# Performance work log

Hardware: AMD Instinct MI355X
Metric: run time of the kernel (lower is better)

## Reference

```python
import jax, jax.numpy as jnp
import numpy as np

B, S, NS, MAX_W, H, NH = 4, 512, 8192, 16, 256, 4
DH = H // NH
FF = 4 * H
NEG = -1e9  # finite mask value; fully-padded spans are zeroed at the end anyway


def _layernorm(x, g, b, eps=1e-5):
    m = jnp.mean(x, -1, keepdims=True)
    v = jnp.var(x, -1, keepdims=True)
    return (x - m) * jax.lax.rsqrt(v + eps) * g + b


def _pos_encoding(n, d):
    pos = np.arange(n)[:, None]
    div = np.exp(np.arange(0, d, 2) * (-np.log(10000.0) / d))
    pe = np.zeros((n, d), np.float32)
    pe[:, 0::2] = np.sin(pos * div)
    pe[:, 1::2] = np.cos(pos * div)
    return jnp.asarray(pe)


def setup_inputs():
    key = jax.random.key(0)
    ks = jax.random.split(key, 12)
    sc = 1.0 / np.sqrt(H)
    starts = jax.random.randint(ks[1], (B, NS), 0, S - MAX_W)
    lengths = jax.random.randint(ks[2], (B, NS), 1, MAX_W + 1)
    return {
        "token_reps": jax.random.normal(ks[0], (B, S, H), jnp.float32),
        "span_ids": jnp.stack([starts, starts + lengths], -1),
        "span_masks": jax.random.uniform(ks[3], (B, NS)) < 0.9,
        "pooling": 1,
        "dummy_query": jax.random.normal(ks[4], (H,), jnp.float32) * sc,
        "w_q": jax.random.normal(ks[5], (H, H), jnp.float32) * sc,
        "w_k": jax.random.normal(ks[6], (H, H), jnp.float32) * sc,
        "w_v": jax.random.normal(ks[7], (H, H), jnp.float32) * sc,
        "b_qkv": jnp.zeros((3, H), jnp.float32),
        "w_o": jax.random.normal(ks[8], (H, H), jnp.float32) * sc,
        "b_o": jnp.zeros((H,), jnp.float32),
        "ln_g": jnp.ones((H,), jnp.float32),
        "ln_b": jnp.zeros((H,), jnp.float32),
        "ffn_w1": jax.random.normal(ks[9], (H, FF), jnp.float32) * sc,
        "ffn_b1": jnp.zeros((FF,), jnp.float32),
        "ffn_w2": jax.random.normal(ks[10], (FF, H), jnp.float32) * (1.0 / np.sqrt(FF)),
        "ffn_b2": jnp.zeros((H,), jnp.float32),
    }


def reference(token_reps, span_ids, span_masks, pooling, dummy_query, w_q, w_k, w_v,
              b_qkv, w_o, b_o, ln_g, ln_b, ffn_w1, ffn_b1, ffn_w2, ffn_b2):
    # sequence positional encoding (eval mode -> dropout is identity)
    tr = token_reps + _pos_encoding(S, H)[None]  # [B,S,H]
    # span lengths, zeroed where span is masked out (as in torch code)
    span_len = (span_ids[:, :, 1] - span_ids[:, :, 0]) * span_masks.astype(span_ids.dtype)  # [B,NS]
    offs = jnp.arange(MAX_W)
    valid = offs[None, None, :] < span_len[:, :, None]  # [B,NS,W] True = real token
    pos = jnp.clip(span_ids[:, :, 0:1] + offs[None, None, :], 0, S - 1)  # [B,NS,W]
    # vectorized ragged gather replacing the python double loop
    x = tr[jnp.arange(B)[:, None, None], pos]  # [B,NS,W,H]
    x = jnp.where(valid[..., None], x, 0.0)
    # single-query multi-head cross attention (dummy query attends over span tokens)
    q = (dummy_query @ w_q.T + b_qkv[0]).reshape(NH, DH)
    k = (x @ w_k.T + b_qkv[1]).reshape(B, NS, MAX_W, NH, DH)
    v = (x @ w_v.T + b_qkv[2]).reshape(B, NS, MAX_W, NH, DH)
    logits = jnp.einsum('hd,bnwhd->bnhw', q, k) / np.sqrt(DH)
    logits = jnp.where(valid[:, :, None, :], logits, NEG)
    attn = jax.nn.softmax(logits, axis=-1)
    ctx = jnp.einsum('bnhw,bnwhd->bnhd', attn, v).reshape(B, NS, H)
    out = ctx @ w_o.T + b_o + dummy_query  # residual with the dummy query
    y = _layernorm(out, ln_g, ln_b)
    f = jax.nn.relu(y @ ffn_w1 + ffn_b1) @ ffn_w2 + ffn_b2
    y = _layernorm(f + y, ln_g, ln_b)
    return jnp.where(span_masks[..., None], y, 0.0)  # [B,NS,H]
```

## Files before the change

### kernel.cpp

```cpp
#include <hip/hip_runtime.h>
#include <hip/hip_bf16.h>

#define B_    4
#define S_    512
#define NS_   8192
#define MAXW  16
#define H_    256
#define NH_   4
#define FF_   1024
#define NSPAN (B_*NS_)
#define NEGV  (-1.0e9f)
#define MT    64
#define LDSK  264

typedef short s16x8 __attribute__((ext_vector_type(8)));
typedef float f32x4 __attribute__((ext_vector_type(4)));

__device__ __forceinline__ unsigned short f2bu(float v){
  __hip_bfloat16 h = __float2bfloat16(v);
  union { __hip_bfloat16 h; unsigned short u; } c; c.h = h; return c.u;
}
__device__ __forceinline__ float bu2f(unsigned short u){
  union { unsigned int i; float f; } c; c.i = ((unsigned int)u) << 16; return c.f;
}
__device__ __forceinline__ f32x4 MFMA(s16x8 a, s16x8 b, f32x4 c){
  return __builtin_amdgcn_mfma_f32_16x16x32_bf16(a, b, c, 0, 0, 0);
}

__global__ __launch_bounds__(256) void prep_q_kernel(
    const float* __restrict__ dq, const float* __restrict__ wq,
    const float* __restrict__ wk, const float* __restrict__ bqkv,
    float* __restrict__ qkvec, float* __restrict__ qb)
{
  __shared__ float q_s[H_];
  const int t = threadIdx.x;
  const int h = blockIdx.x;
  float acc = bqkv[t];
  const float4* wr = (const float4*)(wq + (size_t)t*H_);
  #pragma unroll 8
  for (int c = 0; c < 64; ++c) {
    float4 u = wr[c];
    float4 d = *(const float4*)(dq + c*4);
    acc += u.x*d.x + u.y*d.y + u.z*d.z + u.w*d.w;
  }
  q_s[t] = acc;
  __syncthreads();
  float s = 0.f;
  #pragma unroll 8
  for (int d = 0; d < 64; ++d) s += q_s[h*64 + d] * wk[(size_t)(h*64 + d)*H_ + t];
  qkvec[h*H_ + t] = s;
  if (t < 64) {
    float p = q_s[h*64 + t] * bqkv[H_ + h*64 + t];
    #pragma unroll
    for (int off = 32; off; off >>= 1) p += __shfl_down(p, off);
    if (t == 0) qb[h] = p;
  }
}

__global__ __launch_bounds__(256) void prep_all_kernel(
    const float* __restrict__ tok, const float* __restrict__ qkvec,
    const float* __restrict__ qb,
    const float* __restrict__ wv, const float* __restrict__ wo,
    const float* __restrict__ bqkv, const float* __restrict__ bo,
    const float* __restrict__ dq,
    const float* __restrict__ w1, const float* __restrict__ w2,
    unsigned short* __restrict__ trbf,
    float* __restrict__ lt, unsigned short* __restrict__ wct,
    unsigned short* __restrict__ w1t, unsigned short* __restrict__ w2t,
    float* __restrict__ zbias)
{
  const int blk = blockIdx.x;
  const int t = threadIdx.x;
  if (blk < 2048) {
    __shared__ float red[4][4];
    const int row = blk;
    const int p = row & (S_ - 1);
    float fac = expf((float)((t >> 1)*2) * (-9.210340371976184f / 256.0f));
    float ang = (float)p * fac;
    float pe = (t & 1) ? cosf(ang) : sinf(ang);
    float v = tok[(size_t)row*H_ + t] + pe;
    trbf[(size_t)row*H_ + t] = f2bu(v);
    float p0 = qkvec[t]*v, p1 = qkvec[H_+t]*v, p2 = qkvec[2*H_+t]*v, p3 = qkvec[3*H_+t]*v;
    const int l = t & 63, wv_ = t >> 6;
    #pragma unroll
    for (int m = 1; m < 64; m <<= 1) {
      p0 += __shfl_xor(p0, m); p1 += __shfl_xor(p1, m);
      p2 += __shfl_xor(p2, m); p3 += __shfl_xor(p3, m);
    }
    if (l == 0) { red[wv_][0]=p0; red[wv_][1]=p1; red[wv_][2]=p2; red[wv_][3]=p3; }
    __syncthreads();
    if (t < 4)
      lt[row*NH_ + t] = (red[0][t]+red[1][t]+red[2][t]+red[3][t] + qb[t]) * 0.125f;
  } else if (blk < 3072) {
    int idx = (blk - 2048)*256 + t;
    int n = idx >> 8, k = idx & 255;
    w1t[idx] = f2bu(w1[(size_t)k*FF_ + n]);
  } else if (blk < 4096) {
    int idx = (blk - 3072)*256 + t;
    int n = idx >> 10, k = idx & 1023;
    w2t[idx] = f2bu(w2[(size_t)k*H_ + n]);
  } else if (blk < 4352) {
    __shared__ float wo_s[H_];
    const int i = blk - 4096;
    wo_s[t] = wo[(size_t)i*H_ + t];
    __syncthreads();
    #pragma unroll
    for (int h = 0; h < NH_; ++h) {
      float s = 0.f;
      #pragma unroll 8
      for (int d = 0; d < 64; ++d)
        s += wo_s[h*64 + d] * wv[(size_t)(h*64 + d)*H_ + t];
      wct[(size_t)i*1024 + h*H_ + t] = f2bu(s);
    }
  } else {
    __shared__ float bv_s[H_];
    bv_s[t] = bqkv[2*H_ + t];
    __syncthreads();
    float acc = bo[t] + dq[t];
    const float4* wr = (const float4*)(wo + (size_t)t*H_);
    #pragma unroll 8
    for (int c = 0; c < 64; ++c) {
      float4 u = wr[c];
      acc += u.x*bv_s[c*4] + u.y*bv_s[c*4+1] + u.z*bv_s[c*4+2] + u.w*bv_s[c*4+3];
    }
    zbias[t] = acc;
  }
}

__global__ __launch_bounds__(256) void pool_kernel(
    const unsigned short* __restrict__ trbf,
    const float* __restrict__ lt,
    const int* __restrict__ span_ids, const int* __restrict__ span_masks,
    int span0, unsigned short* __restrict__ pooled)
{
  const int t = threadIdx.x;
  const int l = t & 63;
  const int wv = t >> 6;
  const int spanL = blockIdx.x * 4 + wv;
  const int span  = span0 + spanL;
  const int b  = span >> 13;
  const int st = span_ids[span*2];
  const int en = span_ids[span*2 + 1];
  const int len = span_masks[span] ? (en - st) : 0;

  const int h = l >> 4, w = l & 15;
  int pos = st + w; pos = pos < 0 ? 0 : (pos > S_-1 ? S_-1 : pos);
  float logit = (w < len) ? lt[(b*S_ + pos)*NH_ + h] : NEGV;
  float mx = logit;
  mx = fmaxf(mx, __shfl_xor(mx, 1));
  mx = fmaxf(mx, __shfl_xor(mx, 2));
  mx = fmaxf(mx, __shfl_xor(mx, 4));
  mx = fmaxf(mx, __shfl_xor(mx, 8));
  float e = expf(logit - mx);
  float se = e;
  se += __shfl_xor(se, 1); se += __shfl_xor(se, 2);
  se += __shfl_xor(se, 4); se += __shfl_xor(se, 8);
  const float av = e / se;

  float acc[NH_][4];
  #pragma unroll
  for (int hh = 0; hh < NH_; ++hh)
    #pragma unroll
    for (int j = 0; j < 4; ++j) acc[hh][j] = 0.f;

  const unsigned short* rb = trbf + (size_t)(b*S_)*H_ + l*4;
  #pragma unroll
  for (int w2 = 0; w2 < MAXW; ++w2) {
    int p2 = st + w2; p2 = p2 < 0 ? 0 : (p2 > S_-1 ? S_-1 : p2);
    ushort4 xv = *(const ushort4*)(rb + (size_t)p2*H_);
    float x0 = bu2f(xv.x), x1 = bu2f(xv.y), x2 = bu2f(xv.z), x3 = bu2f(xv.w);
    #pragma unroll
    for (int hh = 0; hh < NH_; ++hh) {
      float a = __shfl(av, hh*16 + w2);
      acc[hh][0] += a*x0; acc[hh][1] += a*x1;
      acc[hh][2] += a*x2; acc[hh][3] += a*x3;
    }
  }
  unsigned short* pp = pooled + (size_t)spanL * 1024;
  #pragma unroll
  for (int hh = 0; hh < NH_; ++hh) {
    ushort4 o;
    o.x = f2bu(acc[hh][0]); o.y = f2bu(acc[hh][1]);
    o.z = f2bu(acc[hh][2]); o.w = f2bu(acc[hh][3]);
    *(ushort4*)(pp + hh*256 + l*4) = o;
  }
}

__device__ __forceinline__ void gemm8(const unsigned short* __restrict__ As,
                                      const unsigned short* __restrict__ bp0,
                                      const unsigned short* __restrict__ bp1,
                                      f32x4 (&ac)[4][2], int ln16, int lg)
{
  s16x8 B0 = *(const s16x8*)bp0;
  s16x8 B1 = *(const s16x8*)bp1;
  #pragma unroll
  for (int s = 0; s < 8; ++s) {
    s16x8 N0 = B0, N1 = B1;
    if (s < 7) { N0 = *(const s16x8*)(bp0 + (s+1)*32); N1 = *(const s16x8*)(bp1 + (s+1)*32); }
    s16x8 a0 = *(const s16x8*)(As + (0*16+ln16)*LDSK + s*32 + lg*8);
    s16x8 a1 = *(const s16x8*)(As + (1*16+ln16)*LDSK + s*32 + lg*8);
    s16x8 a2 = *(const s16x8*)(As + (2*16+ln16)*LDSK + s*32 + lg*8);
    s16x8 a3 = *(const s16x8*)(As + (3*16+ln16)*LDSK + s*32 + lg*8);
    ac[0][0]=MFMA(a0,B0,ac[0][0]); ac[1][0]=MFMA(a1,B0,ac[1][0]);
    ac[2][0]=MFMA(a2,B0,ac[2][0]); ac[3][0]=MFMA(a3,B0,ac[3][0]);
    ac[0][1]=MFMA(a0,B1,ac[0][1]); ac[1][1]=MFMA(a1,B1,ac[1][1]);
    ac[2][1]=MFMA(a2,B1,ac[2][1]); ac[3][1]=MFMA(a3,B1,ac[3][1]);
    B0 = N0; B1 = N1;
  }
}

__global__ __launch_bounds__(512, 4) void fused_gemm_kernel(
    const unsigned short* __restrict__ pooled,
    const unsigned short* __restrict__ wct,
    const float* __restrict__ zbias,
    const unsigned short* __restrict__ w1t, const float* __restrict__ b1,
    const unsigned short* __restrict__ w2t, const float* __restrict__ b2,
    const float* __restrict__ lng, const float* __restrict__ lnb,
    const int* __restrict__ masks, int span0,
    float* __restrict__ out)
{
  __shared__ __align__(16) unsigned short bufA[MT][LDSK];
  __shared__ __align__(16) unsigned short bufB[MT][LDSK];
  __shared__ float part_s[8][MT][2];

  const int t = threadIdx.x;
  const int l = t & 63;
  const int w = t >> 6;
  const int ln16 = l & 15;
  const int lg = l >> 4;
  const int m0l = blockIdx.x * MT;
  const int m0g = span0 + m0l;
  const int ncol = w * 32;

  int srow[4], k8[4];
  #pragma unroll
  for (int q = 0; q < 4; ++q) {
    int idx = q*512 + t;
    srow[q] = idx >> 5;
    k8[q]   = (idx & 31)*8;
  }
  const unsigned short* pbase = pooled + (size_t)m0l*1024;

  f32x4 acc[4][2];
  #pragma unroll
  for (int mf = 0; mf < 4; ++mf){ acc[mf][0]=(f32x4){0,0,0,0}; acc[mf][1]=(f32x4){0,0,0,0}; }

  const unsigned short* bz0 = wct + (size_t)(ncol + ln16)*1024 + lg*8;
  const unsigned short* bz1 = wct + (size_t)(ncol + 16 + ln16)*1024 + lg*8;

  unsigned short* As = &bufA[0][0];
  unsigned short* An = &bufB[0][0];

  uint4 sr[4];
  #pragma unroll
  for (int q = 0; q < 4; ++q)
    sr[q] = *(const uint4*)(pbase + (size_t)srow[q]*1024 + k8[q]);
  #pragma unroll
  for (int q = 0; q < 4; ++q)
    *(uint4*)(As + srow[q]*LDSK + k8[q]) = sr[q];
  __syncthreads();

  s16x8 GA[4], GB[4];
  #define LOADBZ(G, kkg) { \
    G[0] = *(const s16x8*)(bz0 + (kkg)*64);      \
    G[1] = *(const s16x8*)(bz0 + (kkg)*64 + 32); \
    G[2] = *(const s16x8*)(bz1 + (kkg)*64);      \
    G[3] = *(const s16x8*)(bz1 + (kkg)*64 + 32); }
  LOADBZ(GA, 0); LOADBZ(GB, 1);

  auto zstep = [&](s16x8 (&G)[4], int kk, int kkgnext) {
    #pragma unroll
    for (int half = 0; half < 2; ++half) {
      s16x8 a0 = *(const s16x8*)(As + (0*16+ln16)*LDSK + kk*64 + half*32 + lg*8);
      s16x8 a1 = *(const s16x8*)(As + (1*16+ln16)*LDSK + kk*64 + half*32 + lg*8);
      s16x8 a2 = *(const s16x8*)(As + (2*16+ln16)*LDSK + kk*64 + half*32 + lg*8);
      s16x8 a3 = *(const s16x8*)(As + (3*16+ln16)*LDSK + kk*64 + half*32 + lg*8);
      acc[0][0]=MFMA(a0,G[0+half],acc[0][0]); acc[1][0]=MFMA(a1,G[0+half],acc[1][0]);
      acc[2][0]=MFMA(a2,G[0+half],acc[2][0]); acc[3][0]=MFMA(a3,G[0+half],acc[3][0]);
      acc[0][1]=MFMA(a0,G[2+half],acc[0][1]); acc[1][1]=MFMA(a1,G[2+half],acc[1][1]);
      acc[2][1]=MFMA(a2,G[2+half],acc[2][1]); acc[3][1]=MFMA(a3,G[2+half],acc[3][1]);
    }
    if (kkgnext < 16) LOADBZ(G, kkgnext);
  };

  #pragma unroll
  for (int c = 0; c < 4; ++c) {
    if (c < 3) {
      #pragma unroll
      for (int q = 0; q < 4; ++q)
        sr[q] = *(const uint4*)(pbase + (size_t)srow[q]*1024 + (c+1)*256 + k8[q]);
    }
    zstep(GA, 0, c*4 + 2);
    zstep(GB, 1, c*4 + 3);
    zstep(GA, 2, c*4 + 4);
    zstep(GB, 3, c*4 + 5);
    if (c < 3) {
      #pragma unroll
      for (int q = 0; q < 4; ++q)
        *(uint4*)(An + srow[q]*LDSK + k8[q]) = sr[q];
      __syncthreads();
      unsigned short* tmp = As; As = An; An = tmp;
    }
  }
  #undef LOADBZ

  unsigned short* y_s  = &bufB[0][0];
  unsigned short* f1_s = &bufA[0][0];
  {
    const float zb0 = zbias[ncol + ln16],      zb1 = zbias[ncol + 16 + ln16];
    const float g0  = lng[ncol + ln16],        g1  = lng[ncol + 16 + ln16];
    const float bl0 = lnb[ncol + ln16],        bl1 = lnb[ncol + 16 + ln16];
    float vals[4][4][2];
    #pragma unroll
    for (int mf = 0; mf < 4; ++mf)
      #pragma unroll
      for (int r = 0; r < 4; ++r) {
        const int row = mf*16 + lg*4 + r;
        float v0 = acc[mf][0][r] + zb0;
        float v1 = acc[mf][1][r] + zb1;
        vals[mf][r][0] = v0; vals[mf][r][1] = v1;
        float s1 = v0 + v1, s2 = v0*v0 + v1*v1;
        s1 += __shfl_xor(s1,1); s2 += __shfl_xor(s2,1);
        s1 += __shfl_xor(s1,2); s2 += __shfl_xor(s2,2);
        s1 += __shfl_xor(s1,4); s2 += __shfl_xor(s2,4);
        s1 += __shfl_xor(s1,8); s2 += __shfl_xor(s2,8);
        if (ln16 == 0) { part_s[w][row][0] = s1; part_s[w][row][1] = s2; }
      }
    __syncthreads();
    #pragma unroll
    for (int mf = 0; mf < 4; ++mf)
      #pragma unroll
      for (int r = 0; r < 4; ++r) {
        const int row = mf*16 + lg*4 + r;
        float s1 = 0.f, s2 = 0.f;
        #pragma unroll
        for (int j = 0; j < 8; ++j) { s1 += part_s[j][row][0]; s2 += part_s[j][row][1]; }
        float mean = s1 * (1.f/H_);
        float var  = s2 * (1.f/H_) - mean*mean; var = fmaxf(var, 0.f);
        float rstd = rsqrtf(var + 1e-5f);
        y_s[row*LDSK + ncol + ln16]      = f2bu((vals[mf][r][0]-mean)*rstd*g0 + bl0);
        y_s[row*LDSK + ncol + 16 + ln16] = f2bu((vals[mf][r][1]-mean)*rstd*g1 + bl1);
      }
  }
  __syncthreads();

  f32x4 f2acc[4][2];
  #pragma unroll
  for (int mf = 0; mf < 4; ++mf){ f2acc[mf][0]=(f32x4){0,0,0,0}; f2acc[mf][1]=(f32x4){0,0,0,0}; }

  #pragma unroll 1
  for (int nc = 0; nc < 4; ++nc) {
    #pragma unroll
    for (int mf = 0; mf < 4; ++mf){ acc[mf][0]=(f32x4){0,0,0,0}; acc[mf][1]=(f32x4){0,0,0,0}; }
    const unsigned short* b10 = w1t + (size_t)(nc*256 + ncol + ln16)*256 + lg*8;
    const unsigned short* b11 = w1t + (size_t)(nc*256 + ncol + 16 + ln16)*256 + lg*8;
    gemm8(y_s, b10, b11, acc, ln16, lg);
    __syncthreads();
    {
      const float bb0 = b1[nc*256 + ncol + ln16];
      const float bb1 = b1[nc*256 + ncol + 16 + ln16];
      #pragma unroll
      for (int mf = 0; mf < 4; ++mf)
        #pragma unroll
        for (int r = 0; r < 4; ++r) {
          const int row = mf*16 + lg*4 + r;
          f1_s[row*LDSK + ncol + ln16]      = f2bu(fmaxf(acc[mf][0][r] + bb0, 0.f));
          f1_s[row*LDSK + ncol + 16 + ln16] = f2bu(fmaxf(acc[mf][1][r] + bb1, 0.f));
        }
    }
    __syncthreads();
    const unsigned short* b20 = w2t + (size_t)(ncol + ln16)*1024 + nc*256 + lg*8;
    const unsigned short* b21 = w2t + (size_t)(ncol + 16 + ln16)*1024 + nc*256 + lg*8;
    gemm8(f1_s, b20, b21, f2acc, ln16, lg);
  }

  {
    const float b20v = b2[ncol + ln16],   b21v = b2[ncol + 16 + ln16];
    const float g0   = lng[ncol + ln16],  g1   = lng[ncol + 16 + ln16];
    const float bl0  = lnb[ncol + ln16],  bl1  = lnb[ncol + 16 + ln16];
    float vals[4][4][2];
    #pragma unroll
    for (int mf = 0; mf < 4; ++mf)
      #pragma unroll
      for (int r = 0; r < 4; ++r) {
        const int row = mf*16 + lg*4 + r;
        float v0 = f2acc[mf][0][r] + b20v + bu2f(y_s[row*LDSK + ncol + ln16]);
        float v1 = f2acc[mf][1][r] + b21v + bu2f(y_s[row*LDSK + ncol + 16 + ln16]);
        vals[mf][r][0] = v0; vals[mf][r][1] = v1;
        float s1 = v0 + v1, s2 = v0*v0 + v1*v1;
        s1 += __shfl_xor(s1,1); s2 += __shfl_xor(s2,1);
        s1 += __shfl_xor(s1,2); s2 += __shfl_xor(s2,2);
        s1 += __shfl_xor(s1,4); s2 += __shfl_xor(s2,4);
        s1 += __shfl_xor(s1,8); s2 += __shfl_xor(s2,8);
        if (ln16 == 0) { part_s[w][row][0] = s1; part_s[w][row][1] = s2; }
      }
    __syncthreads();
    #pragma unroll
    for (int mf = 0; mf < 4; ++mf)
      #pragma unroll
      for (int r = 0; r < 4; ++r) {
        const int row = mf*16 + lg*4 + r;
        const int span = m0g + row;
        float s1 = 0.f, s2 = 0.f;
        #pragma unroll
        for (int j = 0; j < 8; ++j) { s1 += part_s[j][row][0]; s2 += part_s[j][row][1]; }
        float mean = s1 * (1.f/H_);
        float var  = s2 * (1.f/H_) - mean*mean; var = fmaxf(var, 0.f);
        float rstd = rsqrtf(var + 1e-5f);
        int mk = masks[span];
        float o0 = (vals[mf][r][0]-mean)*rstd*g0 + bl0;
        float o1 = (vals[mf][r][1]-mean)*rstd*g1 + bl1;
        out[(size_t)span*H_ + ncol + ln16]      = mk ? o0 : 0.f;
        out[(size_t)span*H_ + ncol + 16 + ln16] = mk ? o1 : 0.f;
      }
  }
}

extern "C" void kernel_launch(void* const* d_in, const int* in_sizes, int n_in,
                              void* d_out, int out_size, void* d_ws, size_t ws_size,
                              hipStream_t stream) {
  const float* tok      = (const float*)d_in[0];
  const int* span_ids   = (const int*)d_in[1];
  const int* span_masks = (const int*)d_in[2];
  const float* dq   = (const float*)d_in[4];
  const float* wq   = (const float*)d_in[5];
  const float* wk   = (const float*)d_in[6];
  const float* wv   = (const float*)d_in[7];
  const float* bqkv = (const float*)d_in[8];
  const float* wo   = (const float*)d_in[9];
  const float* bo   = (const float*)d_in[10];
  const float* lng  = (const float*)d_in[11];
  const float* lnb  = (const float*)d_in[12];
  const float* w1   = (const float*)d_in[13];
  const float* b1   = (const float*)d_in[14];
  const float* w2   = (const float*)d_in[15];
  const float* b2   = (const float*)d_in[16];

  float* ws    = (float*)d_ws;
  float* qkvec = ws;
  float* qbuf  = qkvec + 1024;
  float* lt    = qbuf + 8;
  float* zbias = lt + 8192;
  unsigned short* ub = (unsigned short*)(zbias + 256);
  unsigned short* trbf = ub;
  unsigned short* wct  = trbf + 524288;
  unsigned short* w1t  = wct + 262144;
  unsigned short* w2t  = w1t + 262144;
  unsigned short* pooled = w2t + 262144;

  const size_t fixed_bytes = (size_t)(1024 + 8 + 8192 + 256)*4
                           + (size_t)(524288 + 262144*3)*2;
  int nb = 1;
  while (nb < 16 && fixed_bytes + (size_t)(NSPAN/nb)*1024*2 > ws_size) nb <<= 1;
  const int spans_b = NSPAN / nb;

  hipLaunchKernelGGL(prep_q_kernel, dim3(NH_), dim3(256), 0, stream,
                     dq, wq, wk, bqkv, qkvec, qbuf);
  hipLaunchKernelGGL(prep_all_kernel, dim3(4353), dim3(256), 0, stream,
                     tok, qkvec, qbuf, wv, wo, bqkv, bo, dq, w1, w2,
                     trbf, lt, wct, w1t, w2t, zbias);

  for (int bi = 0; bi < nb; ++bi) {
    const int span0 = bi * spans_b;
    hipLaunchKernelGGL(pool_kernel, dim3(spans_b/4), dim3(256), 0, stream,
                       trbf, lt, span_ids, span_masks, span0, pooled);
    hipLaunchKernelGGL(fused_gemm_kernel, dim3(spans_b/MT), dim3(512), 0, stream,
                       pooled, wct, zbias, w1t, b1, w2t, b2,
                       lng, lnb, span_masks, span0, (float*)d_out);
  }
}
```

Before: 175.6 us.

## Fuse span attention pooling into the fused GEMM kernel via shared memory

Removes the separate pool kernel and its global pooled buffer of 32768x1024 bf16. Each GEMM block now computes the per-span softmax weights and the attention-weighted token sums for two heads at a time straight into shared memory, then runs the Wct GEMM on them. This removes a global write and read of the pooled intermediate, plus a kernel launch and any batching loop. In exchange the GEMM block does extra gather work with more syncs, and shared memory use grows, which may lower occupancy.

```diff
diff --git a/kernel.cpp b/kernel.cpp
--- a/kernel.cpp
+++ b/kernel.cpp
@@ -127,65 +127,6 @@
   }
 }
 
-__global__ __launch_bounds__(256) void pool_kernel(
-    const unsigned short* __restrict__ trbf,
-    const float* __restrict__ lt,
-    const int* __restrict__ span_ids, const int* __restrict__ span_masks,
-    int span0, unsigned short* __restrict__ pooled)
-{
-  const int t = threadIdx.x;
-  const int l = t & 63;
-  const int wv = t >> 6;
-  const int spanL = blockIdx.x * 4 + wv;
-  const int span  = span0 + spanL;
-  const int b  = span >> 13;
-  const int st = span_ids[span*2];
-  const int en = span_ids[span*2 + 1];
-  const int len = span_masks[span] ? (en - st) : 0;
-
-  const int h = l >> 4, w = l & 15;
-  int pos = st + w; pos = pos < 0 ? 0 : (pos > S_-1 ? S_-1 : pos);
-  float logit = (w < len) ? lt[(b*S_ + pos)*NH_ + h] : NEGV;
-  float mx = logit;
-  mx = fmaxf(mx, __shfl_xor(mx, 1));
-  mx = fmaxf(mx, __shfl_xor(mx, 2));
-  mx = fmaxf(mx, __shfl_xor(mx, 4));
-  mx = fmaxf(mx, __shfl_xor(mx, 8));
-  float e = expf(logit - mx);
-  float se = e;
-  se += __shfl_xor(se, 1); se += __shfl_xor(se, 2);
-  se += __shfl_xor(se, 4); se += __shfl_xor(se, 8);
-  const float av = e / se;
-
-  float acc[NH_][4];
-  #pragma unroll
-  for (int hh = 0; hh < NH_; ++hh)
-    #pragma unroll
-    for (int j = 0; j < 4; ++j) acc[hh][j] = 0.f;
-
-  const unsigned short* rb = trbf + (size_t)(b*S_)*H_ + l*4;
-  #pragma unroll
-  for (int w2 = 0; w2 < MAXW; ++w2) {
-    int p2 = st + w2; p2 = p2 < 0 ? 0 : (p2 > S_-1 ? S_-1 : p2);
-    ushort4 xv = *(const ushort4*)(rb + (size_t)p2*H_);
-    float x0 = bu2f(xv.x), x1 = bu2f(xv.y), x2 = bu2f(xv.z), x3 = bu2f(xv.w);
-    #pragma unroll
-    for (int hh = 0; hh < NH_; ++hh) {
-      float a = __shfl(av, hh*16 + w2);
-      acc[hh][0] += a*x0; acc[hh][1] += a*x1;
-      acc[hh][2] += a*x2; acc[hh][3] += a*x3;
-    }
-  }
-  unsigned short* pp = pooled + (size_t)spanL * 1024;
-  #pragma unroll
-  for (int hh = 0; hh < NH_; ++hh) {
-    ushort4 o;
-    o.x = f2bu(acc[hh][0]); o.y = f2bu(acc[hh][1]);
-    o.z = f2bu(acc[hh][2]); o.w = f2bu(acc[hh][3]);
-    *(ushort4*)(pp + hh*256 + l*4) = o;
-  }
-}
-
 __device__ __forceinline__ void gemm8(const unsigned short* __restrict__ As,
                                       const unsigned short* __restrict__ bp0,
                                       const unsigned short* __restrict__ bp1,
@@ -210,106 +151,119 @@
 }
 
 __global__ __launch_bounds__(512, 4) void fused_gemm_kernel(
-    const unsigned short* __restrict__ pooled,
-    const unsigned short* __restrict__ wct,
-    const float* __restrict__ zbias,
+    const unsigned short* __restrict__ trbf, const float* __restrict__ lt,
+    const int* __restrict__ span_ids, const int* __restrict__ span_masks,
+    const unsigned short* __restrict__ wct, const float* __restrict__ zbias,
     const unsigned short* __restrict__ w1t, const float* __restrict__ b1,
     const unsigned short* __restrict__ w2t, const float* __restrict__ b2,
     const float* __restrict__ lng, const float* __restrict__ lnb,
-    const int* __restrict__ masks, int span0,
     float* __restrict__ out)
 {
-  __shared__ __align__(16) unsigned short bufA[MT][LDSK];
-  __shared__ __align__(16) unsigned short bufB[MT][LDSK];
-  __shared__ float part_s[8][MT][2];
+  __shared__ __align__(16) unsigned short bufA[MT*LDSK];
+  __shared__ __align__(16) unsigned short bufB[MT*LDSK];
+  __shared__ __align__(16) float scratch[2048];
+  __shared__ int meta_rb[MT];
+  __shared__ int meta_len[MT];
+  __shared__ int meta_mk[MT];
+
+  float (*attn_s)[MT][16] = (float(*)[MT][16])scratch;
+  float (*part_s)[MT][2]  = (float(*)[MT][2])scratch;
 
   const int t = threadIdx.x;
   const int l = t & 63;
   const int w = t >> 6;
   const int ln16 = l & 15;
   const int lg = l >> 4;
-  const int m0l = blockIdx.x * MT;
-  const int m0g = span0 + m0l;
+  const int m0 = blockIdx.x * MT;
   const int ncol = w * 32;
 
-  int srow[4], k8[4];
-  #pragma unroll
-  for (int q = 0; q < 4; ++q) {
-    int idx = q*512 + t;
-    srow[q] = idx >> 5;
-    k8[q]   = (idx & 31)*8;
-  }
-  const unsigned short* pbase = pooled + (size_t)m0l*1024;
+  if (t < MT) {
+    int gs = m0 + t;
+    int st = span_ids[gs*2];
+    int en = span_ids[gs*2 + 1];
+    int mk = span_masks[gs];
+    meta_rb[t]  = (gs >> 13) * S_ + st;
+    meta_len[t] = mk ? (en - st) : 0;
+    meta_mk[t]  = mk;
+  }
+  __syncthreads();
+
+  auto attn_pass = [&](int p){
+    #pragma unroll
+    for (int q = 0; q < 4; ++q) {
+      int slot = q*512 + t;
+      int w16 = slot & 15;
+      int sp  = (slot >> 4) & 63;
+      int h2  = slot >> 10;
+      int rb  = meta_rb[sp];
+      int len = meta_len[sp];
+      float lg_ = (w16 < len) ? lt[(rb + w16)*NH_ + p*2 + h2] : NEGV;
+      float mx = lg_;
+      mx = fmaxf(mx, __shfl_xor(mx,1));
+      mx = fmaxf(mx, __shfl_xor(mx,2));
+      mx = fmaxf(mx, __shfl_xor(mx,4));
+      mx = fmaxf(mx, __shfl_xor(mx,8));
+      float e = expf(lg_ - mx);
+      float se = e;
+      se += __shfl_xor(se,1); se += __shfl_xor(se,2);
+      se += __shfl_xor(se,4); se += __shfl_xor(se,8);
+      attn_s[h2][sp][w16] = e / se;
+    }
+  };
+
+  auto pool_pass = [&](){
+    #pragma unroll 1
+    for (int i = 0; i < 8; ++i) {
+      int sp = w*8 + i;
+      int rb = meta_rb[sp];
+      const ushort4* p4 = (const ushort4*)(trbf + (size_t)rb*H_) + l;
+      float a0=0,a1=0,a2=0,a3=0, q0=0,q1=0,q2=0,q3=0;
+      #pragma unroll
+      for (int w2 = 0; w2 < MAXW; ++w2) {
+        ushort4 xv = p4[w2*64];
+        float av0 = attn_s[0][sp][w2];
+        float av1 = attn_s[1][sp][w2];
+        float x0=bu2f(xv.x), x1=bu2f(xv.y), x2=bu2f(xv.z), x3=bu2f(xv.w);
+        a0 += av0*x0; a1 += av0*x1; a2 += av0*x2; a3 += av0*x3;
+        q0 += av1*x0; q1 += av1*x1; q2 += av1*x2; q3 += av1*x3;
+      }
+      ushort4 o0, o1;
+      o0.x=f2bu(a0); o0.y=f2bu(a1); o0.z=f2bu(a2); o0.w=f2bu(a3);
+      o1.x=f2bu(q0); o1.y=f2bu(q1); o1.z=f2bu(q2); o1.w=f2bu(q3);
+      *(ushort4*)(bufA + sp*LDSK + l*4) = o0;
+      *(ushort4*)(bufB + sp*LDSK + l*4) = o1;
+    }
+  };
+
+  const int col0 = ncol + ln16, col1 = ncol + 16 + ln16;
 
   f32x4 acc[4][2];
   #pragma unroll
   for (int mf = 0; mf < 4; ++mf){ acc[mf][0]=(f32x4){0,0,0,0}; acc[mf][1]=(f32x4){0,0,0,0}; }
 
-  const unsigned short* bz0 = wct + (size_t)(ncol + ln16)*1024 + lg*8;
-  const unsigned short* bz1 = wct + (size_t)(ncol + 16 + ln16)*1024 + lg*8;
-
-  unsigned short* As = &bufA[0][0];
-  unsigned short* An = &bufB[0][0];
-
-  uint4 sr[4];
-  #pragma unroll
-  for (int q = 0; q < 4; ++q)
-    sr[q] = *(const uint4*)(pbase + (size_t)srow[q]*1024 + k8[q]);
-  #pragma unroll
-  for (int q = 0; q < 4; ++q)
-    *(uint4*)(As + srow[q]*LDSK + k8[q]) = sr[q];
-  __syncthreads();
-
-  s16x8 GA[4], GB[4];
-  #define LOADBZ(G, kkg) { \
-    G[0] = *(const s16x8*)(bz0 + (kkg)*64);      \
-    G[1] = *(const s16x8*)(bz0 + (kkg)*64 + 32); \
-    G[2] = *(const s16x8*)(bz1 + (kkg)*64);      \
-    G[3] = *(const s16x8*)(bz1 + (kkg)*64 + 32); }
-  LOADBZ(GA, 0); LOADBZ(GB, 1);
-
-  auto zstep = [&](s16x8 (&G)[4], int kk, int kkgnext) {
-    #pragma unroll
-    for (int half = 0; half < 2; ++half) {
-      s16x8 a0 = *(const s16x8*)(As + (0*16+ln16)*LDSK + kk*64 + half*32 + lg*8);
-      s16x8 a1 = *(const s16x8*)(As + (1*16+ln16)*LDSK + kk*64 + half*32 + lg*8);
-      s16x8 a2 = *(const s16x8*)(As + (2*16+ln16)*LDSK + kk*64 + half*32 + lg*8);
-      s16x8 a3 = *(const s16x8*)(As + (3*16+ln16)*LDSK + kk*64 + half*32 + lg*8);
-      acc[0][0]=MFMA(a0,G[0+half],acc[0][0]); acc[1][0]=MFMA(a1,G[0+half],acc[1][0]);
-      acc[2][0]=MFMA(a2,G[0+half],acc[2][0]); acc[3][0]=MFMA(a3,G[0+half],acc[3][0]);
-      acc[0][1]=MFMA(a0,G[2+half],acc[0][1]); acc[1][1]=MFMA(a1,G[2+half],acc[1][1]);
-      acc[2][1]=MFMA(a2,G[2+half],acc[2][1]); acc[3][1]=MFMA(a3,G[2+half],acc[3][1]);
-    }
-    if (kkgnext < 16) LOADBZ(G, kkgnext);
-  };
-
-  #pragma unroll
-  for (int c = 0; c < 4; ++c) {
-    if (c < 3) {
-      #pragma unroll
-      for (int q = 0; q < 4; ++q)
-        sr[q] = *(const uint4*)(pbase + (size_t)srow[q]*1024 + (c+1)*256 + k8[q]);
-    }
-    zstep(GA, 0, c*4 + 2);
-    zstep(GB, 1, c*4 + 3);
-    zstep(GA, 2, c*4 + 4);
-    zstep(GB, 3, c*4 + 5);
-    if (c < 3) {
-      #pragma unroll
-      for (int q = 0; q < 4; ++q)
-        *(uint4*)(An + srow[q]*LDSK + k8[q]) = sr[q];
-      __syncthreads();
-      unsigned short* tmp = As; As = An; An = tmp;
-    }
-  }
-  #undef LOADBZ
-
-  unsigned short* y_s  = &bufB[0][0];
-  unsigned short* f1_s = &bufA[0][0];
+  attn_pass(0);
+  __syncthreads();
+  pool_pass();
+  __syncthreads();
+  attn_pass(1);
+  gemm8(bufA, wct + (size_t)col0*1024 + 0*256 + lg*8,
+               wct + (size_t)col1*1024 + 0*256 + lg*8, acc, ln16, lg);
+  gemm8(bufB, wct + (size_t)col0*1024 + 1*256 + lg*8,
+               wct + (size_t)col1*1024 + 1*256 + lg*8, acc, ln16, lg);
+  __syncthreads();
+  pool_pass();
+  __syncthreads();
+  gemm8(bufA, wct + (size_t)col0*1024 + 2*256 + lg*8,
+               wct + (size_t)col1*1024 + 2*256 + lg*8, acc, ln16, lg);
+  gemm8(bufB, wct + (size_t)col0*1024 + 3*256 + lg*8,
+               wct + (size_t)col1*1024 + 3*256 + lg*8, acc, ln16, lg);
+
+  unsigned short* y_s  = bufB;
+  unsigned short* f1_s = bufA;
   {
-    const float zb0 = zbias[ncol + ln16],      zb1 = zbias[ncol + 16 + ln16];
-    const float g0  = lng[ncol + ln16],        g1  = lng[ncol + 16 + ln16];
-    const float bl0 = lnb[ncol + ln16],        bl1 = lnb[ncol + 16 + ln16];
+    const float zb0 = zbias[col0], zb1 = zbias[col1];
+    const float g0  = lng[col0],   g1  = lng[col1];
+    const float bl0 = lnb[col0],   bl1 = lnb[col1];
     float vals[4][4][2];
     #pragma unroll
     for (int mf = 0; mf < 4; ++mf)
@@ -338,8 +292,8 @@
         float mean = s1 * (1.f/H_);
         float var  = s2 * (1.f/H_) - mean*mean; var = fmaxf(var, 0.f);
         float rstd = rsqrtf(var + 1e-5f);
-        y_s[row*LDSK + ncol + ln16]      = f2bu((vals[mf][r][0]-mean)*rstd*g0 + bl0);
-        y_s[row*LDSK + ncol + 16 + ln16] = f2bu((vals[mf][r][1]-mean)*rstd*g1 + bl1);
+        y_s[row*LDSK + col0] = f2bu((vals[mf][r][0]-mean)*rstd*g0 + bl0);
+        y_s[row*LDSK + col1] = f2bu((vals[mf][r][1]-mean)*rstd*g1 + bl1);
       }
   }
   __syncthreads();
@@ -352,40 +306,40 @@
   for (int nc = 0; nc < 4; ++nc) {
     #pragma unroll
     for (int mf = 0; mf < 4; ++mf){ acc[mf][0]=(f32x4){0,0,0,0}; acc[mf][1]=(f32x4){0,0,0,0}; }
-    const unsigned short* b10 = w1t + (size_t)(nc*256 + ncol + ln16)*256 + lg*8;
-    const unsigned short* b11 = w1t + (size_t)(nc*256 + ncol + 16 + ln16)*256 + lg*8;
+    const unsigned short* b10 = w1t + (size_t)(nc*256 + col0)*256 + lg*8;
+    const unsigned short* b11 = w1t + (size_t)(nc*256 + col1)*256 + lg*8;
     gemm8(y_s, b10, b11, acc, ln16, lg);
     __syncthreads();
     {
-      const float bb0 = b1[nc*256 + ncol + ln16];
-      const float bb1 = b1[nc*256 + ncol + 16 + ln16];
+      const float bb0 = b1[nc*256 + col0];
+      const float bb1 = b1[nc*256 + col1];
       #pragma unroll
       for (int mf = 0; mf < 4; ++mf)
         #pragma unroll
         for (int r = 0; r < 4; ++r) {
           const int row = mf*16 + lg*4 + r;
-          f1_s[row*LDSK + ncol + ln16]      = f2bu(fmaxf(acc[mf][0][r] + bb0, 0.f));
-          f1_s[row*LDSK + ncol + 16 + ln16] = f2bu(fmaxf(acc[mf][1][r] + bb1, 0.f));
+          f1_s[row*LDSK + col0] = f2bu(fmaxf(acc[mf][0][r] + bb0, 0.f));
+          f1_s[row*LDSK + col1] = f2bu(fmaxf(acc[mf][1][r] + bb1, 0.f));
         }
     }
     __syncthreads();
-    const unsigned short* b20 = w2t + (size_t)(ncol + ln16)*1024 + nc*256 + lg*8;
-    const unsigned short* b21 = w2t + (size_t)(ncol + 16 + ln16)*1024 + nc*256 + lg*8;
+    const unsigned short* b20 = w2t + (size_t)col0*1024 + nc*256 + lg*8;
+    const unsigned short* b21 = w2t + (size_t)col1*1024 + nc*256 + lg*8;
     gemm8(f1_s, b20, b21, f2acc, ln16, lg);
   }
 
   {
-    const float b20v = b2[ncol + ln16],   b21v = b2[ncol + 16 + ln16];
-    const float g0   = lng[ncol + ln16],  g1   = lng[ncol + 16 + ln16];
-    const float bl0  = lnb[ncol + ln16],  bl1  = lnb[ncol + 16 + ln16];
+    const float b20v = b2[col0],  b21v = b2[col1];
+    const float g0   = lng[col0], g1   = lng[col1];
+    const float bl0  = lnb[col0], bl1  = lnb[col1];
     float vals[4][4][2];
     #pragma unroll
     for (int mf = 0; mf < 4; ++mf)
       #pragma unroll
       for (int r = 0; r < 4; ++r) {
         const int row = mf*16 + lg*4 + r;
-        float v0 = f2acc[mf][0][r] + b20v + bu2f(y_s[row*LDSK + ncol + ln16]);
-        float v1 = f2acc[mf][1][r] + b21v + bu2f(y_s[row*LDSK + ncol + 16 + ln16]);
+        float v0 = f2acc[mf][0][r] + b20v + bu2f(y_s[row*LDSK + col0]);
+        float v1 = f2acc[mf][1][r] + b21v + bu2f(y_s[row*LDSK + col1]);
         vals[mf][r][0] = v0; vals[mf][r][1] = v1;
         float s1 = v0 + v1, s2 = v0*v0 + v1*v1;
         s1 += __shfl_xor(s1,1); s2 += __shfl_xor(s2,1);
@@ -400,18 +354,18 @@
       #pragma unroll
       for (int r = 0; r < 4; ++r) {
         const int row = mf*16 + lg*4 + r;
-        const int span = m0g + row;
+        const int span = m0 + row;
         float s1 = 0.f, s2 = 0.f;
         #pragma unroll
         for (int j = 0; j < 8; ++j) { s1 += part_s[j][row][0]; s2 += part_s[j][row][1]; }
         float mean = s1 * (1.f/H_);
         float var  = s2 * (1.f/H_) - mean*mean; var = fmaxf(var, 0.f);
         float rstd = rsqrtf(var + 1e-5f);
-        int mk = masks[span];
+        int mk = meta_mk[row];
         float o0 = (vals[mf][r][0]-mean)*rstd*g0 + bl0;
         float o1 = (vals[mf][r][1]-mean)*rstd*g1 + bl1;
-        out[(size_t)span*H_ + ncol + ln16]      = mk ? o0 : 0.f;
-        out[(size_t)span*H_ + ncol + 16 + ln16] = mk ? o1 : 0.f;
+        out[(size_t)span*H_ + col0] = mk ? o0 : 0.f;
+        out[(size_t)span*H_ + col1] = mk ? o1 : 0.f;
       }
   }
 }
@@ -446,26 +400,13 @@
   unsigned short* wct  = trbf + 524288;
   unsigned short* w1t  = wct + 262144;
   unsigned short* w2t  = w1t + 262144;
-  unsigned short* pooled = w2t + 262144;
-
-  const size_t fixed_bytes = (size_t)(1024 + 8 + 8192 + 256)*4
-                           + (size_t)(524288 + 262144*3)*2;
-  int nb = 1;
-  while (nb < 16 && fixed_bytes + (size_t)(NSPAN/nb)*1024*2 > ws_size) nb <<= 1;
-  const int spans_b = NSPAN / nb;
 
   hipLaunchKernelGGL(prep_q_kernel, dim3(NH_), dim3(256), 0, stream,
                      dq, wq, wk, bqkv, qkvec, qbuf);
   hipLaunchKernelGGL(prep_all_kernel, dim3(4353), dim3(256), 0, stream,
                      tok, qkvec, qbuf, wv, wo, bqkv, bo, dq, w1, w2,
                      trbf, lt, wct, w1t, w2t, zbias);
-
-  for (int bi = 0; bi < nb; ++bi) {
-    const int span0 = bi * spans_b;
-    hipLaunchKernelGGL(pool_kernel, dim3(spans_b/4), dim3(256), 0, stream,
-                       trbf, lt, span_ids, span_masks, span0, pooled);
-    hipLaunchKernelGGL(fused_gemm_kernel, dim3(spans_b/MT), dim3(512), 0, stream,
-                       pooled, wct, zbias, w1t, b1, w2t, b2,
-                       lng, lnb, span_masks, span0, (float*)d_out);
-  }
-}
+  hipLaunchKernelGGL(fused_gemm_kernel, dim3(NSPAN/MT), dim3(512), 0, stream,
+                     trbf, lt, span_ids, span_masks, wct, zbias,
+                     w1t, b1, w2t, b2, lng, lnb, (float*)d_out);
+}
```

Result: slower. 270.2 us (+53.9%).
